# Kernel tuning notes

Hardware: AMD Instinct MI355X
Metric: run time of the kernel (lower is better)

Reference implementation:

```python
import jax, jax.numpy as jnp
import numpy as np

D = 128      # d_model
H = 8        # nhead
DFF = 256    # dim_feedforward
S = 1000     # num sets
L = 90       # set size
N = S * L    # total tokens (lidar voxels + image patches)
VN = 45000   # voxel_num (lidar tokens)


def _ln(x, g, b, eps=1e-5):
    m = x.mean(-1, keepdims=True)
    v = ((x - m) ** 2).mean(-1, keepdims=True)
    return (x - m) / jnp.sqrt(v + eps) * g + b


def setup_inputs() -> dict:
    key = jax.random.key(0)
    ks = jax.random.split(key, 16)
    p = lambda k, sh: jax.random.normal(k, sh, jnp.float32) * 0.02
    inp = {
        "src": jax.random.normal(ks[0], (N, D), jnp.float32),
        "pos": jax.random.normal(ks[1], (N, D), jnp.float32),
        # every token appears exactly once across all sets (permutation)
        "set_voxel_inds": jax.random.permutation(ks[2], N).reshape(S, L).astype(jnp.int32),
        "set_voxel_masks": jnp.zeros((S, L), bool),
        "voxel_num": VN,
        # nn.MultiheadAttention params
        "in_proj_w": p(ks[3], (3 * D, D)), "in_proj_b": jnp.zeros((3 * D,), jnp.float32),
        "out_w": p(ks[4], (D, D)), "out_b": jnp.zeros((D,), jnp.float32),
        # image-branch FFN + norms
        "lin1_w": p(ks[5], (DFF, D)), "lin1_b": jnp.zeros((DFF,), jnp.float32),
        "lin2_w": p(ks[6], (D, DFF)), "lin2_b": jnp.zeros((D,), jnp.float32),
        "n1_g": jnp.ones((D,), jnp.float32), "n1_b": jnp.zeros((D,), jnp.float32),
        "n2_g": jnp.ones((D,), jnp.float32), "n2_b": jnp.zeros((D,), jnp.float32),
        # lidar-branch FFN + norms (split_ffn=True)
        "l_lin1_w": p(ks[7], (DFF, D)), "l_lin1_b": jnp.zeros((DFF,), jnp.float32),
        "l_lin2_w": p(ks[8], (D, DFF)), "l_lin2_b": jnp.zeros((D,), jnp.float32),
        "ln1_g": jnp.ones((D,), jnp.float32), "ln1_b": jnp.zeros((D,), jnp.float32),
        "ln2_g": jnp.ones((D,), jnp.float32), "ln2_b": jnp.zeros((D,), jnp.float32),
        # encoder-layer output norm
        "enc_g": jnp.ones((D,), jnp.float32), "enc_b": jnp.zeros((D,), jnp.float32),
    }
    return inp


def reference(src, pos, set_voxel_inds, set_voxel_masks, voxel_num,
              in_proj_w, in_proj_b, out_w, out_b,
              lin1_w, lin1_b, lin2_w, lin2_b, n1_g, n1_b, n2_g, n2_b,
              l_lin1_w, l_lin1_b, l_lin2_w, l_lin2_b, ln1_g, ln1_b, ln2_g, ln2_b,
              enc_g, enc_b):
    identity = src
    Sx, Lx = set_voxel_inds.shape
    d = src.shape[-1]
    dh = d // H

    # ---- gather sets ----
    sf = src[set_voxel_inds]              # [S, L, D]
    sp = pos[set_voxel_inds]              # [S, L, D]
    q = sf + sp
    k = sf + sp
    v = sf

    # ---- nn.MultiheadAttention (batch_first, eval mode) ----
    qp = q @ in_proj_w[:d].T + in_proj_b[:d]
    kp = k @ in_proj_w[d:2 * d].T + in_proj_b[d:2 * d]
    vp = v @ in_proj_w[2 * d:].T + in_proj_b[2 * d:]
    qh = qp.reshape(Sx, Lx, H, dh)
    kh = kp.reshape(Sx, Lx, H, dh)
    vh = vp.reshape(Sx, Lx, H, dh)
    scale = 1.0 / np.sqrt(dh).astype(np.float32)
    scores = jnp.einsum('sqhd,skhd->shqk', qh, kh) * scale
    scores = scores + jnp.where(set_voxel_masks[:, None, None, :], -1e9, 0.0)
    attn = jax.nn.softmax(scores, axis=-1)
    o = jnp.einsum('shqk,skhd->sqhd', attn, vh).reshape(Sx, Lx, d)
    src2 = o @ out_w.T + out_b            # [S, L, D]

    # ---- scatter back to per-token order (first-occurrence via flip trick) ----
    flat = set_voxel_inds.reshape(-1)
    ar = jnp.arange(flat.shape[0], dtype=flat.dtype)
    perm = jnp.zeros((src.shape[0],), flat.dtype).at[flat[::-1]].set(ar[::-1])
    src2 = src2.reshape(-1, d)[perm]      # [N, D]

    # ---- split FFN (lidar first voxel_num tokens, image rest) ----
    x = src + src2
    x = jnp.concatenate([_ln(x[:voxel_num], ln1_g, ln1_b),
                         _ln(x[voxel_num:], n1_g, n1_b)], axis=0)
    fl = jax.nn.relu(x[:voxel_num] @ l_lin1_w.T + l_lin1_b) @ l_lin2_w.T + l_lin2_b
    fi = jax.nn.relu(x[voxel_num:] @ lin1_w.T + lin1_b) @ lin2_w.T + lin2_b
    x = x + jnp.concatenate([fl, fi], axis=0)
    x = jnp.concatenate([_ln(x[:voxel_num], ln2_g, ln2_b),
                         _ln(x[voxel_num:], n2_g, n2_b)], axis=0)

    # ---- UniTR_EncoderLayer residual + final norm ----
    return _ln(x + identity, enc_g, enc_b)
```

## Files before the change

kernel.cpp:

```cpp
#include <hip/hip_runtime.h>
#include <hip/hip_bf16.h>
#include <cmath>

#define N_TOK 90000
#define DM 128
#define NH 8
#define DH 16
#define NS 1000
#define LS 90
#define LSP 96
#define DFF 256
#define VN 45000
#define NB_L 704
#define NB_I 704

typedef __attribute__((ext_vector_type(8))) short short8;
typedef __attribute__((ext_vector_type(4))) short short4_t;
typedef __attribute__((ext_vector_type(4))) float f32x4;

#define SWZ(row, byte) ((byte) ^ (((row) & 7) << 4))

__device__ __forceinline__ unsigned short f2bf(float f) {
  __hip_bfloat16 h = __float2bfloat16(f);
  union { __hip_bfloat16 h; unsigned short u; } c; c.h = h; return c.u;
}
__device__ __forceinline__ float bf2f(unsigned short u) {
  union { unsigned short u; __hip_bfloat16 h; } c; c.u = u; return __bfloat162float(c.h);
}

__global__ __launch_bounds__(256) void k_wconv(
    const float* __restrict__ a0, const float* __restrict__ a1,
    const float* __restrict__ a2, const float* __restrict__ a3,
    const float* __restrict__ a4, const float* __restrict__ a5,
    unsigned short* __restrict__ dst)
{
  int c = blockIdx.x * 256 + threadIdx.x;
  const float* s; int base, kkn, K;
  if      (c <  6144) { s = a0; base = 0;     kkn = 4; K = 128; }
  else if (c <  8192) { s = a1; base = 6144;  kkn = 4; K = 128; }
  else if (c < 12288) { s = a2; base = 8192;  kkn = 4; K = 128; }
  else if (c < 16384) { s = a3; base = 12288; kkn = 4; K = 128; }
  else if (c < 20480) { s = a4; base = 16384; kkn = 8; K = 256; }
  else                { s = a5; base = 20480; kkn = 8; K = 256; }
  int lc = c - base;
  int nt = lc / (kkn * 64);
  int rem = lc - nt * (kkn * 64);
  int kk = rem >> 6, l = rem & 63;
  int row = nt * 16 + (l & 15);
  int col = kk * 32 + (l >> 4) * 8;
  const float* sp = s + (size_t)row * K + col;
  short8 o;
  #pragma unroll
  for (int e = 0; e < 8; e++) o[e] = (short)f2bf(sp[e]);
  *(short8*)&dst[(size_t)c * 8] = o;
}

__global__ __launch_bounds__(512, 4) void k_set(
    const float* __restrict__ src, const float* __restrict__ pos,
    const int* __restrict__ inds, const unsigned char* __restrict__ masks,
    const unsigned short* __restrict__ Wq, const float* __restrict__ bq_,
    const unsigned short* __restrict__ Wo, const float* __restrict__ bo,
    const float* __restrict__ lg, const float* __restrict__ lb,
    const float* __restrict__ ig, const float* __restrict__ ib,
    unsigned short* __restrict__ x1)
{
  __shared__ __align__(16) char QKV[2 * LSP * 256 + 128 * 200];
  __shared__ float bias[LSP];
  __shared__ int tok[LSP];
  const int s = blockIdx.x;
  const int tid = threadIdx.x;
  const int w = tid >> 6, l = tid & 63;
  const int g = l >> 4, cb = l & 15;

  if (tid < LSP) {
    tok[tid] = inds[s * LS + ((tid < LS) ? tid : 0)];
    bias[tid] = (tid < LS && !masks[s * LS + tid]) ? 0.f : -1e9f;
  }
  __syncthreads();

  char* Qd = QKV;
  char* Kd = QKV + LSP * 256;
  char* Vt = QKV + 2 * LSP * 256;

  if (w < 6) {
    const int row = w * 16 + cb;
    const int t = tok[row];
    short8 bq[4], bv[4];
    #pragma unroll
    for (int kk = 0; kk < 4; kk++) {
      const float* sp = &src[(size_t)t * DM + kk * 32 + g * 8];
      const float* pp = &pos[(size_t)t * DM + kk * 32 + g * 8];
      float4 s0 = *(const float4*)sp, s1 = *(const float4*)(sp + 4);
      float4 p0 = *(const float4*)pp, p1 = *(const float4*)(pp + 4);
      short8 q, v;
      q[0] = (short)f2bf(s0.x + p0.x); q[1] = (short)f2bf(s0.y + p0.y);
      q[2] = (short)f2bf(s0.z + p0.z); q[3] = (short)f2bf(s0.w + p0.w);
      q[4] = (short)f2bf(s1.x + p1.x); q[5] = (short)f2bf(s1.y + p1.y);
      q[6] = (short)f2bf(s1.z + p1.z); q[7] = (short)f2bf(s1.w + p1.w);
      v[0] = (short)f2bf(s0.x); v[1] = (short)f2bf(s0.y);
      v[2] = (short)f2bf(s0.z); v[3] = (short)f2bf(s0.w);
      v[4] = (short)f2bf(s1.x); v[5] = (short)f2bf(s1.y);
      v[6] = (short)f2bf(s1.z); v[7] = (short)f2bf(s1.w);
      bq[kk] = q; bv[kk] = v;
    }

    short8 A0[4];
    {
      const unsigned short* wb = Wq + (size_t)l * 8;
      #pragma unroll
      for (int kk = 0; kk < 4; kk++) A0[kk] = *(const short8*)(wb + kk * 512);
    }
    #pragma unroll
    for (int nt = 0; nt < 24; nt++) {
      short8 An[4];
      if (nt < 23) {
        const unsigned short* wb = Wq + ((size_t)(nt + 1) * 256 + l) * 8;
        #pragma unroll
        for (int kk = 0; kk < 4; kk++) An[kk] = *(const short8*)(wb + kk * 512);
      }
      f32x4 acc = {0.f, 0.f, 0.f, 0.f};
      if (nt < 16) {
        #pragma unroll
        for (int kk = 0; kk < 4; kk++)
          acc = __builtin_amdgcn_mfma_f32_16x16x32_bf16(A0[kk], bq[kk], acc, 0, 0, 0);
      } else {
        #pragma unroll
        for (int kk = 0; kk < 4; kk++)
          acc = __builtin_amdgcn_mfma_f32_16x16x32_bf16(A0[kk], bv[kk], acc, 0, 0, 0);
      }
      float4 bb = *(const float4*)&bq_[nt * 16 + g * 4];
      if (nt < 16) {
        char* base = (nt < 8) ? Qd : Kd;
        const int colb = (nt & 7) * 16 + g * 4;
        short4_t o;
        o[0] = (short)f2bf(acc[0] + bb.x); o[1] = (short)f2bf(acc[1] + bb.y);
        o[2] = (short)f2bf(acc[2] + bb.z); o[3] = (short)f2bf(acc[3] + bb.w);
        *(short4_t*)(base + SWZ(row, row * 256 + colb * 2)) = o;
      } else {
        float bba[4] = {bb.x, bb.y, bb.z, bb.w};
        #pragma unroll
        for (int j = 0; j < 4; j++) {
          int ch = (nt - 16) * 16 + g * 4 + j;
          *(unsigned short*)(Vt + ch * 200 + row * 2) = f2bf(acc[j] + bba[j]);
        }
      }
      #pragma unroll
      for (int kk = 0; kk < 4; kk++) A0[kk] = An[kk];
    }
  }
  __syncthreads();

  {
    const int hb = w * 32;
    float bi[6][4];
    #pragma unroll
    for (int kt = 0; kt < 6; kt++)
      #pragma unroll
      for (int r = 0; r < 4; r++)
        bi[kt][r] = bias[kt * 16 + g * 4 + r];

    short8 aK[6];
    #pragma unroll
    for (int kt = 0; kt < 6; kt++) {
      short8 v = {0, 0, 0, 0, 0, 0, 0, 0};
      int key = kt * 16 + cb;
      if (g < 2) v = *(const short8*)(Kd + SWZ(key, key * 256 + hb + g * 16));
      aK[kt] = v;
    }
    short8 aV[3];
    #pragma unroll
    for (int kb = 0; kb < 3; kb++) {
      const char* vr = Vt + (w * 16 + cb) * 200;
      short4_t lo = *(const short4_t*)(vr + (kb * 32 + g * 4) * 2);
      short4_t hi = *(const short4_t*)(vr + (kb * 32 + 16 + g * 4) * 2);
      short8 v;
      v[0] = lo[0]; v[1] = lo[1]; v[2] = lo[2]; v[3] = lo[3];
      v[4] = hi[0]; v[5] = hi[1]; v[6] = hi[2]; v[7] = hi[3];
      aV[kb] = v;
    }

    #pragma unroll
    for (int qt = 0; qt < 6; qt++) {
      const int qi = qt * 16 + cb;
      short8 aQ = {0, 0, 0, 0, 0, 0, 0, 0};
      if (g < 2) aQ = *(const short8*)(Qd + SWZ(qi, qi * 256 + hb + g * 16));

      f32x4 acc[6];
      #pragma unroll
      for (int kt = 0; kt < 6; kt++) {
        f32x4 z = {0.f, 0.f, 0.f, 0.f};
        acc[kt] = __builtin_amdgcn_mfma_f32_16x16x32_bf16(aK[kt], aQ, z, 0, 0, 0);
      }
      #pragma unroll
      for (int kt = 0; kt < 6; kt++)
        #pragma unroll
        for (int r = 0; r < 4; r++)
          acc[kt][r] = acc[kt][r] * 0.25f + bi[kt][r];
      float mx = -1e30f;
      #pragma unroll
      for (int kt = 0; kt < 6; kt++)
        #pragma unroll
        for (int r = 0; r < 4; r++) mx = fmaxf(mx, acc[kt][r]);
      mx = fmaxf(mx, __shfl_xor(mx, 16));
      mx = fmaxf(mx, __shfl_xor(mx, 32));
      float sm = 0.f;
      #pragma unroll
      for (int kt = 0; kt < 6; kt++)
        #pragma unroll
        for (int r = 0; r < 4; r++) {
          acc[kt][r] = __expf(acc[kt][r] - mx);
          sm += acc[kt][r];
        }
      sm += __shfl_xor(sm, 16);
      sm += __shfl_xor(sm, 32);
      const float inv = 1.f / sm;
      short8 P[3];
      #pragma unroll
      for (int kb = 0; kb < 3; kb++) {
        short8 p;
        #pragma unroll
        for (int e = 0; e < 8; e++) {
          int kt = kb * 2 + (e >> 2);
          p[e] = (short)f2bf(acc[kt][e & 3] * inv);
        }
        P[kb] = p;
      }
      f32x4 accO = {0.f, 0.f, 0.f, 0.f};
      #pragma unroll
      for (int kb = 0; kb < 3; kb++)
        accO = __builtin_amdgcn_mfma_f32_16x16x32_bf16(aV[kb], P[kb], accO, 0, 0, 0);
      if (qi < LS) {
        short4_t o;
        #pragma unroll
        for (int r = 0; r < 4; r++) o[r] = (short)f2bf(accO[r]);
        *(short4_t*)(Qd + SWZ(qi, qi * 256 + hb + g * 8)) = o;
      }
    }
  }
  __syncthreads();

  if (w < 6) {
    const int row = w * 16 + cb;
    const bool ok = row < LS;
    const int t = tok[row];
    short8 bf[4];
    #pragma unroll
    for (int kk = 0; kk < 4; kk++)
      bf[kk] = *(const short8*)(Qd + SWZ(row, row * 256 + kk * 64 + g * 16));

    f32x4 acc[8];
    short8 A0[4];
    {
      const unsigned short* wb = Wo + (size_t)l * 8;
      #pragma unroll
      for (int kk = 0; kk < 4; kk++) A0[kk] = *(const short8*)(wb + kk * 512);
    }
    #pragma unroll
    for (int nt = 0; nt < 8; nt++) {
      short8 An[4];
      if (nt < 7) {
        const unsigned short* wb = Wo + ((size_t)(nt + 1) * 256 + l) * 8;
        #pragma unroll
        for (int kk = 0; kk < 4; kk++) An[kk] = *(const short8*)(wb + kk * 512);
      }
      f32x4 c = {0.f, 0.f, 0.f, 0.f};
      #pragma unroll
      for (int kk = 0; kk < 4; kk++)
        c = __builtin_amdgcn_mfma_f32_16x16x32_bf16(A0[kk], bf[kk], c, 0, 0, 0);
      acc[nt] = c;
      #pragma unroll
      for (int kk = 0; kk < 4; kk++) A0[kk] = An[kk];
    }

    float ta[8][4]; float ssum = 0.f;
    #pragma unroll
    for (int nt = 0; nt < 8; nt++) {
      float4 bo4 = *(const float4*)&bo[nt * 16 + g * 4];
      float4 sv  = *(const float4*)&src[(size_t)t * DM + nt * 16 + g * 4];
      ta[nt][0] = acc[nt][0] + bo4.x + sv.x;
      ta[nt][1] = acc[nt][1] + bo4.y + sv.y;
      ta[nt][2] = acc[nt][2] + bo4.z + sv.z;
      ta[nt][3] = acc[nt][3] + bo4.w + sv.w;
      ssum += ta[nt][0] + ta[nt][1] + ta[nt][2] + ta[nt][3];
    }
    ssum += __shfl_xor(ssum, 16); ssum += __shfl_xor(ssum, 32);
    const float mean = ssum * (1.f / 128.f);
    float vv = 0.f;
    #pragma unroll
    for (int nt = 0; nt < 8; nt++)
      #pragma unroll
      for (int j = 0; j < 4; j++) { float d = ta[nt][j] - mean; vv += d * d; }
    vv += __shfl_xor(vv, 16); vv += __shfl_xor(vv, 32);
    const float rstd = rsqrtf(vv * (1.f / 128.f) + 1e-5f);
    const bool lidar = t < VN;
    const float* gp = lidar ? lg : ig;
    const float* bp = lidar ? lb : ib;
    #pragma unroll
    for (int nt = 0; nt < 8; nt++) {
      float4 g4 = *(const float4*)&gp[nt * 16 + g * 4];
      float4 b4 = *(const float4*)&bp[nt * 16 + g * 4];
      short4_t o;
      o[0] = (short)f2bf((ta[nt][0] - mean) * rstd * g4.x + b4.x);
      o[1] = (short)f2bf((ta[nt][1] - mean) * rstd * g4.y + b4.y);
      o[2] = (short)f2bf((ta[nt][2] - mean) * rstd * g4.z + b4.z);
      o[3] = (short)f2bf((ta[nt][3] - mean) * rstd * g4.w + b4.w);
      if (ok) *(short4_t*)&x1[(size_t)t * DM + nt * 16 + g * 4] = o;
    }
  }
}

__global__ __launch_bounds__(256) void k_ffn(
    const unsigned short* __restrict__ x1, const float* __restrict__ src,
    const unsigned short* __restrict__ W1l, const float* __restrict__ B1l,
    const unsigned short* __restrict__ W1i, const float* __restrict__ B1i,
    const unsigned short* __restrict__ W2l, const float* __restrict__ B2l,
    const unsigned short* __restrict__ W2i, const float* __restrict__ B2i,
    const float* __restrict__ lg2, const float* __restrict__ lbb2,
    const float* __restrict__ ig2, const float* __restrict__ ibb2,
    const float* __restrict__ eg, const float* __restrict__ eb,
    float* __restrict__ out)
{
  __shared__ __align__(16) unsigned short hid[64 * 256];
  const int tid = threadIdx.x;
  const int w = tid >> 6, l = tid & 63;
  const int g = l >> 4, cb = l & 15;
  const bool lid = blockIdx.x < NB_L;
  const int t0 = lid ? blockIdx.x * 64 : VN + (blockIdx.x - NB_L) * 64;
  const int limit = lid ? VN : N_TOK;
  const unsigned short* W1 = lid ? W1l : W1i;
  const float* B1 = lid ? B1l : B1i;
  const unsigned short* W2 = lid ? W2l : W2i;
  const float* B2 = lid ? B2l : B2i;
  const float* g2  = lid ? lg2  : ig2;
  const float* bb2 = lid ? lbb2 : ibb2;

  const int row = w * 16 + cb;
  const int t = t0 + row;
  const int tc = (t < limit) ? t : (limit - 1);
  const bool ok = t < limit;

  short8 b1[4];
  #pragma unroll
  for (int kk = 0; kk < 4; kk++)
    b1[kk] = *(const short8*)&x1[(size_t)tc * DM + kk * 32 + g * 8];

  for (int nt = 0; nt < 16; nt++) {
    const unsigned short* wbase = W1 + ((size_t)nt * 256 + l) * 8;
    short8 A[4];
    #pragma unroll
    for (int kk = 0; kk < 4; kk++) A[kk] = *(const short8*)(wbase + kk * 512);
    f32x4 acc = {0.f, 0.f, 0.f, 0.f};
    #pragma unroll
    for (int kk = 0; kk < 4; kk++)
      acc = __builtin_amdgcn_mfma_f32_16x16x32_bf16(A[kk], b1[kk], acc, 0, 0, 0);
    float4 bb = *(const float4*)&B1[nt * 16 + g * 4];
    short4_t h;
    h[0] = (short)f2bf(fmaxf(acc[0] + bb.x, 0.f));
    h[1] = (short)f2bf(fmaxf(acc[1] + bb.y, 0.f));
    h[2] = (short)f2bf(fmaxf(acc[2] + bb.z, 0.f));
    h[3] = (short)f2bf(fmaxf(acc[3] + bb.w, 0.f));
    *(short4_t*)((char*)hid + SWZ(row, row * 512 + nt * 32 + g * 8)) = h;
  }

  short8 b2[8];
  #pragma unroll
  for (int kk = 0; kk < 8; kk++)
    b2[kk] = *(const short8*)((const char*)hid + SWZ(row, row * 512 + kk * 64 + g * 16));

  f32x4 acc2[8];
  for (int nt = 0; nt < 8; nt++) {
    const unsigned short* wbase = W2 + ((size_t)nt * 512 + l) * 8;
    short8 A[8];
    #pragma unroll
    for (int kk = 0; kk < 8; kk++) A[kk] = *(const short8*)(wbase + kk * 512);
    f32x4 c = {0.f, 0.f, 0.f, 0.f};
    #pragma unroll
    for (int kk = 0; kk < 8; kk++)
      c = __builtin_amdgcn_mfma_f32_16x16x32_bf16(A[kk], b2[kk], c, 0, 0, 0);
    acc2[nt] = c;
  }

  float ta[8][4]; float s = 0.f;
  #pragma unroll
  for (int nt = 0; nt < 8; nt++) {
    short4_t xv = *(const short4_t*)&x1[(size_t)tc * DM + nt * 16 + g * 4];
    float4 bb = *(const float4*)&B2[nt * 16 + g * 4];
    ta[nt][0] = bf2f((unsigned short)xv[0]) + acc2[nt][0] + bb.x;
    ta[nt][1] = bf2f((unsigned short)xv[1]) + acc2[nt][1] + bb.y;
    ta[nt][2] = bf2f((unsigned short)xv[2]) + acc2[nt][2] + bb.z;
    ta[nt][3] = bf2f((unsigned short)xv[3]) + acc2[nt][3] + bb.w;
    s += ta[nt][0] + ta[nt][1] + ta[nt][2] + ta[nt][3];
  }
  s += __shfl_xor(s, 16); s += __shfl_xor(s, 32);
  const float mean = s * (1.f / 128.f);
  float vv = 0.f;
  #pragma unroll
  for (int nt = 0; nt < 8; nt++)
    #pragma unroll
    for (int j = 0; j < 4; j++) { float d = ta[nt][j] - mean; vv += d * d; }
  vv += __shfl_xor(vv, 16); vv += __shfl_xor(vv, 32);
  const float rstd = rsqrtf(vv * (1.f / 128.f) + 1e-5f);

  float za[8][4]; float s2 = 0.f;
  #pragma unroll
  for (int nt = 0; nt < 8; nt++) {
    float4 g4 = *(const float4*)&g2[nt * 16 + g * 4];
    float4 b4 = *(const float4*)&bb2[nt * 16 + g * 4];
    float4 sv = *(const float4*)&src[(size_t)tc * DM + nt * 16 + g * 4];
    za[nt][0] = (ta[nt][0] - mean) * rstd * g4.x + b4.x + sv.x;
    za[nt][1] = (ta[nt][1] - mean) * rstd * g4.y + b4.y + sv.y;
    za[nt][2] = (ta[nt][2] - mean) * rstd * g4.z + b4.z + sv.z;
    za[nt][3] = (ta[nt][3] - mean) * rstd * g4.w + b4.w + sv.w;
    s2 += za[nt][0] + za[nt][1] + za[nt][2] + za[nt][3];
  }
  s2 += __shfl_xor(s2, 16); s2 += __shfl_xor(s2, 32);
  const float mean2 = s2 * (1.f / 128.f);
  float vv2 = 0.f;
  #pragma unroll
  for (int nt = 0; nt < 8; nt++)
    #pragma unroll
    for (int j = 0; j < 4; j++) { float d = za[nt][j] - mean2; vv2 += d * d; }
  vv2 += __shfl_xor(vv2, 16); vv2 += __shfl_xor(vv2, 32);
  const float rstd2 = rsqrtf(vv2 * (1.f / 128.f) + 1e-5f);

  #pragma unroll
  for (int nt = 0; nt < 8; nt++) {
    float4 e4 = *(const float4*)&eg[nt * 16 + g * 4];
    float4 eb4 = *(const float4*)&eb[nt * 16 + g * 4];
    float4 o;
    o.x = (za[nt][0] - mean2) * rstd2 * e4.x + eb4.x;
    o.y = (za[nt][1] - mean2) * rstd2 * e4.y + eb4.y;
    o.z = (za[nt][2] - mean2) * rstd2 * e4.z + eb4.z;
    o.w = (za[nt][3] - mean2) * rstd2 * e4.w + eb4.w;
    if (ok) *(float4*)&out[(size_t)t * DM + nt * 16 + g * 4] = o;
  }
}

extern "C" void kernel_launch(void* const* d_in, const int* in_sizes, int n_in,
                              void* d_out, int out_size, void* d_ws, size_t ws_size,
                              hipStream_t stream) {
  (void)in_sizes; (void)n_in; (void)out_size;
  const float* src  = (const float*)d_in[0];
  const float* pos  = (const float*)d_in[1];
  const int*   inds = (const int*)d_in[2];
  const unsigned char* masks = (const unsigned char*)d_in[3];
  const float* Wqkv = (const float*)d_in[5];
  const float* bqkv = (const float*)d_in[6];
  const float* Wo   = (const float*)d_in[7];
  const float* bo   = (const float*)d_in[8];
  const float* lin1_w = (const float*)d_in[9];
  const float* lin1_b = (const float*)d_in[10];
  const float* lin2_w = (const float*)d_in[11];
  const float* lin2_b = (const float*)d_in[12];
  const float* n1_g = (const float*)d_in[13];
  const float* n1_b = (const float*)d_in[14];
  const float* n2_g = (const float*)d_in[15];
  const float* n2_b = (const float*)d_in[16];
  const float* l_lin1_w = (const float*)d_in[17];
  const float* l_lin1_b = (const float*)d_in[18];
  const float* l_lin2_w = (const float*)d_in[19];
  const float* l_lin2_b = (const float*)d_in[20];
  const float* ln1_g = (const float*)d_in[21];
  const float* ln1_b = (const float*)d_in[22];
  const float* ln2_g = (const float*)d_in[23];
  const float* ln2_b = (const float*)d_in[24];
  const float* enc_g = (const float*)d_in[25];
  const float* enc_b = (const float*)d_in[26];

  const size_t buf = (size_t)N_TOK * DM;
  if (ws_size < (buf + 196608) * sizeof(unsigned short)) return;
  unsigned short* x1  = (unsigned short*)d_ws;
  unsigned short* Wbf = x1 + buf;
  unsigned short* WbQKV = Wbf;
  unsigned short* WbO   = Wbf + 6144  * 8;
  unsigned short* Wb1L  = Wbf + 8192  * 8;
  unsigned short* Wb1I  = Wbf + 12288 * 8;
  unsigned short* Wb2L  = Wbf + 16384 * 8;
  unsigned short* Wb2I  = Wbf + 20480 * 8;

  k_wconv<<<96, 256, 0, stream>>>(Wqkv, Wo, l_lin1_w, lin1_w, l_lin2_w, lin2_w, Wbf);
  k_set<<<NS, 512, 0, stream>>>(src, pos, inds, masks, WbQKV, bqkv, WbO, bo,
                                ln1_g, ln1_b, n1_g, n1_b, x1);
  k_ffn<<<NB_L + NB_I, 256, 0, stream>>>(x1, src,
                                         Wb1L, l_lin1_b, Wb1I, lin1_b,
                                         Wb2L, l_lin2_b, Wb2I, lin2_b,
                                         ln2_g, ln2_b, n2_g, n2_b,
                                         enc_g, enc_b, (float*)d_out);
}
```

Before: 132.3 us.

## Alias Q buffer over V-transpose region to cut LDS and raise occupancy

Computes K and V projections first, loads V fragments into registers, then reuses the V-transpose LDS region for Q. This drops shared memory per block by a Q-sized buffer, and launch bounds are raised from 4 to 6 blocks per SM to exploit the lower LDS footprint. It adds an extra barrier and keeps bq and aV live in registers across phases, which may raise register pressure and force spills at the tighter launch bound.

```diff
diff --git a/kernel.cpp b/kernel.cpp
--- a/kernel.cpp
+++ b/kernel.cpp
@@ -55,7 +55,7 @@
   *(short8*)&dst[(size_t)c * 8] = o;
 }
 
-__global__ __launch_bounds__(512, 4) void k_set(
+__global__ __launch_bounds__(512, 6) void k_set(
     const float* __restrict__ src, const float* __restrict__ pos,
     const int* __restrict__ inds, const unsigned char* __restrict__ masks,
     const unsigned short* __restrict__ Wq, const float* __restrict__ bq_,
@@ -64,7 +64,7 @@
     const float* __restrict__ ig, const float* __restrict__ ib,
     unsigned short* __restrict__ x1)
 {
-  __shared__ __align__(16) char QKV[2 * LSP * 256 + 128 * 200];
+  __shared__ __align__(16) char QKV[LSP * 256 + 128 * 200];
   __shared__ float bias[LSP];
   __shared__ int tok[LSP];
   const int s = blockIdx.x;
@@ -78,14 +78,16 @@
   }
   __syncthreads();
 
-  char* Qd = QKV;
-  char* Kd = QKV + LSP * 256;
-  char* Vt = QKV + 2 * LSP * 256;
+  char* Kd = QKV;
+  char* Vt = QKV + LSP * 256;
+  char* Qd = QKV + LSP * 256;
+
+  const int row = w * 16 + cb;
+  short8 bq[4];
 
   if (w < 6) {
-    const int row = w * 16 + cb;
     const int t = tok[row];
-    short8 bq[4], bv[4];
+    short8 bv[4];
     #pragma unroll
     for (int kk = 0; kk < 4; kk++) {
       const float* sp = &src[(size_t)t * DM + kk * 32 + g * 8];
@@ -106,12 +108,12 @@
 
     short8 A0[4];
     {
-      const unsigned short* wb = Wq + (size_t)l * 8;
+      const unsigned short* wb = Wq + ((size_t)8 * 256 + l) * 8;
       #pragma unroll
       for (int kk = 0; kk < 4; kk++) A0[kk] = *(const short8*)(wb + kk * 512);
     }
     #pragma unroll
-    for (int nt = 0; nt < 24; nt++) {
+    for (int nt = 8; nt < 24; nt++) {
       short8 An[4];
       if (nt < 23) {
         const unsigned short* wb = Wq + ((size_t)(nt + 1) * 256 + l) * 8;
@@ -130,12 +132,11 @@
       }
       float4 bb = *(const float4*)&bq_[nt * 16 + g * 4];
       if (nt < 16) {
-        char* base = (nt < 8) ? Qd : Kd;
         const int colb = (nt & 7) * 16 + g * 4;
         short4_t o;
         o[0] = (short)f2bf(acc[0] + bb.x); o[1] = (short)f2bf(acc[1] + bb.y);
         o[2] = (short)f2bf(acc[2] + bb.z); o[3] = (short)f2bf(acc[3] + bb.w);
-        *(short4_t*)(base + SWZ(row, row * 256 + colb * 2)) = o;
+        *(short4_t*)(Kd + SWZ(row, row * 256 + colb * 2)) = o;
       } else {
         float bba[4] = {bb.x, bb.y, bb.z, bb.w};
         #pragma unroll
@@ -144,6 +145,50 @@
           *(unsigned short*)(Vt + ch * 200 + row * 2) = f2bf(acc[j] + bba[j]);
         }
       }
+      #pragma unroll
+      for (int kk = 0; kk < 4; kk++) A0[kk] = An[kk];
+    }
+  }
+  __syncthreads();
+
+  short8 aV[3];
+  #pragma unroll
+  for (int kb = 0; kb < 3; kb++) {
+    const char* vr = Vt + (w * 16 + cb) * 200;
+    short4_t lo = *(const short4_t*)(vr + (kb * 32 + g * 4) * 2);
+    short4_t hi = *(const short4_t*)(vr + (kb * 32 + 16 + g * 4) * 2);
+    short8 v;
+    v[0] = lo[0]; v[1] = lo[1]; v[2] = lo[2]; v[3] = lo[3];
+    v[4] = hi[0]; v[5] = hi[1]; v[6] = hi[2]; v[7] = hi[3];
+    aV[kb] = v;
+  }
+  __syncthreads();
+
+  if (w < 6) {
+    short8 A0[4];
+    {
+      const unsigned short* wb = Wq + (size_t)l * 8;
+      #pragma unroll
+      for (int kk = 0; kk < 4; kk++) A0[kk] = *(const short8*)(wb + kk * 512);
+    }
+    #pragma unroll
+    for (int nt = 0; nt < 8; nt++) {
+      short8 An[4];
+      if (nt < 7) {
+        const unsigned short* wb = Wq + ((size_t)(nt + 1) * 256 + l) * 8;
+        #pragma unroll
+        for (int kk = 0; kk < 4; kk++) An[kk] = *(const short8*)(wb + kk * 512);
+      }
+      f32x4 acc = {0.f, 0.f, 0.f, 0.f};
+      #pragma unroll
+      for (int kk = 0; kk < 4; kk++)
+        acc = __builtin_amdgcn_mfma_f32_16x16x32_bf16(A0[kk], bq[kk], acc, 0, 0, 0);
+      float4 bb = *(const float4*)&bq_[nt * 16 + g * 4];
+      const int colb = nt * 16 + g * 4;
+      short4_t o;
+      o[0] = (short)f2bf(acc[0] + bb.x); o[1] = (short)f2bf(acc[1] + bb.y);
+      o[2] = (short)f2bf(acc[2] + bb.z); o[3] = (short)f2bf(acc[3] + bb.w);
+      *(short4_t*)(Qd + SWZ(row, row * 256 + colb * 2)) = o;
       #pragma unroll
       for (int kk = 0; kk < 4; kk++) A0[kk] = An[kk];
     }
@@ -166,17 +211,6 @@
       int key = kt * 16 + cb;
       if (g < 2) v = *(const short8*)(Kd + SWZ(key, key * 256 + hb + g * 16));
       aK[kt] = v;
-    }
-    short8 aV[3];
-    #pragma unroll
-    for (int kb = 0; kb < 3; kb++) {
-      const char* vr = Vt + (w * 16 + cb) * 200;
-      short4_t lo = *(const short4_t*)(vr + (kb * 32 + g * 4) * 2);
-      short4_t hi = *(const short4_t*)(vr + (kb * 32 + 16 + g * 4) * 2);
-      short8 v;
-      v[0] = lo[0]; v[1] = lo[1]; v[2] = lo[2]; v[3] = lo[3];
-      v[4] = hi[0]; v[5] = hi[1]; v[6] = hi[2]; v[7] = hi[3];
-      aV[kb] = v;
     }
 
     #pragma unroll
@@ -240,7 +274,6 @@
   __syncthreads();
 
   if (w < 6) {
-    const int row = w * 16 + cb;
     const bool ok = row < LS;
     const int t = tok[row];
     short8 bf[4];
```

Measured after the change: 186.1 us. 40.7% more time.
